# Kernel tuning notes

Measured on AMD Instinct MI355X. Metric: run time of the kernel, lower is better.

The kernel has to match this reference:

```python
import jax, jax.numpy as jnp
import numpy as np

N_NODES = 100000


def _mean_agg(x, src, dst, n_nodes):
    # gather neighbor (src) features, segment-sum into destination nodes, divide by in-degree
    summed = jax.ops.segment_sum(x[src], dst, num_segments=n_nodes)  # [N, d]
    deg = jax.ops.segment_sum(jnp.ones_like(dst, dtype=x.dtype), dst, num_segments=n_nodes)
    return summed / jnp.clip(deg, 1.0)[:, None]  # DGL clamps zero in-degree to 1


def _sage_conv(x, src, dst, W_self, W_neigh, b, n_nodes):
    h_neigh = _mean_agg(x, src, dst, n_nodes)
    # DGL SAGEConv(mean): fc_self(h_self) + fc_neigh(h_neigh); single bias
    return x @ W_self + h_neigh @ W_neigh + b


def setup_inputs() -> dict:
    key = jax.random.key(0)
    ks = jax.random.split(key, 8)
    in_f, hid_f, out_f = 64, 64, 16
    n_edges = 1200000
    return {
        "x": jax.random.normal(ks[0], (N_NODES, in_f), dtype=jnp.float32),
        "src": jax.random.randint(ks[1], (n_edges,), 0, N_NODES),
        "dst": jax.random.randint(ks[2], (n_edges,), 0, N_NODES),
        "W1_self": jax.random.normal(ks[3], (in_f, hid_f), dtype=jnp.float32) / np.sqrt(in_f),
        "W1_neigh": jax.random.normal(ks[4], (in_f, hid_f), dtype=jnp.float32) / np.sqrt(in_f),
        "b1": jnp.zeros((hid_f,), dtype=jnp.float32),
        "W2_self": jax.random.normal(ks[5], (hid_f, out_f), dtype=jnp.float32) / np.sqrt(hid_f),
        "W2_neigh": jax.random.normal(ks[6], (hid_f, out_f), dtype=jnp.float32) / np.sqrt(hid_f),
        "b2": jnp.zeros((out_f,), dtype=jnp.float32),
    }


def reference(x, src, dst, W1_self, W1_neigh, b1, W2_self, W2_neigh, b2):
    h = _sage_conv(x, src, dst, W1_self, W1_neigh, b1, N_NODES)
    h = jax.nn.relu(h)
    h = _sage_conv(h, src, dst, W2_self, W2_neigh, b2, N_NODES)
    return h
```

## Files before the change

### kernel.cpp

```cpp
#include <hip/hip_runtime.h>

#define N_NODES 100000
#define N_EDGES 1200000
#define BK 64
#define NB 1563
#define CHUNK_E 4096
#define NBLK_E 293
#define TOT_H (NB * NBLK_E)
#define NSB2 ((TOT_H + 1023) / 1024)
#define CAP 1536
#define ND1 3125

#define OFF_ROWPTR 0
#define OFF_HISTG  401408
#define OFF_BLK2   2234368
#define OFF_PAIRS  2236416
#define OFF_SORTED 7036928
#define OFF_Y1     11837440
#define OFF_H1     24637440

typedef __attribute__((ext_vector_type(8))) short short8;
typedef __attribute__((ext_vector_type(4))) float f32x4;

__device__ __forceinline__ unsigned short f2bf(float f) {
    unsigned u = __float_as_uint(f);
    unsigned r = (u + 0x7fffu + ((u >> 16) & 1u)) >> 16;
    return (unsigned short)r;
}

__global__ __launch_bounds__(256) void wtrans_kernel(
    const float* __restrict__ Wn, unsigned short* __restrict__ wt)
{
    const int t = threadIdx.x;
#pragma unroll
    for (int i = 0; i < 16; ++i) {
        const int e = t + i * 256;
        wt[(e & 63) * 64 + (e >> 6)] = f2bf(Wn[e]);
    }
}

__global__ __launch_bounds__(256) void hist_dense1_kernel(
    const int* __restrict__ dst, int* __restrict__ hist_g,
    const float* __restrict__ x,
    const unsigned short* __restrict__ wt,
    const float* __restrict__ Ws, const float* __restrict__ b,
    unsigned short* __restrict__ y1, float* __restrict__ z1)
{
    __shared__ float sx[32 * 64];
    __shared__ unsigned short sxbf[32 * 64];
    const int t = threadIdx.x;

    if (blockIdx.x < NBLK_E) {
        int* h = (int*)sx;
        const int e0 = blockIdx.x * CHUNK_E;
        const int e1 = min(e0 + CHUNK_E, N_EDGES);
        for (int i = t; i < NB; i += 256) h[i] = 0;
        __syncthreads();
        for (int e = e0 + t; e < e1; e += 256)
            atomicAdd(&h[dst[e] >> 6], 1);
        __syncthreads();
        for (int i = t; i < NB; i += 256)
            hist_g[i * NBLK_E + blockIdx.x] = h[i];
        return;
    }

    const int bid = blockIdx.x - NBLK_E;
    const int w = t >> 6;
    const int lane = t & 63;
    const int chunk = bid * 32;

    {
        const float4* gx = (const float4*)(x + (size_t)chunk * 64);
        float4* sx4 = (float4*)sx;
#pragma unroll
        for (int i = 0; i < 2; ++i) {
            const int fidx = t + i * 256;
            const float4 v = gx[fidx];
            sx4[fidx] = v;
            const int r = fidx >> 4;
            const int f = fidx & 15;
            const int cs = (f >> 1) ^ (r & 7);
            uint2 p;
            p.x = (unsigned)f2bf(v.x) | ((unsigned)f2bf(v.y) << 16);
            p.y = (unsigned)f2bf(v.z) | ((unsigned)f2bf(v.w) << 16);
            *(uint2*)((char*)sxbf + r * 128 + cs * 16 + (f & 1) * 8) = p;
        }
    }
    __syncthreads();

    if (w >= 2) {
        const int nsub = (w & 1) * 16;
        float wr[64];
#pragma unroll
        for (int k = 0; k < 64; ++k) wr[k] = Ws[k * 64 + lane];
        const float bj = b[lane];
#pragma unroll 1
        for (int m = 0; m < 16; ++m) {
            const int node = nsub + m;
            const float4* xr = (const float4*)(sx + node * 64);
            float a0 = 0.f, a1 = 0.f, a2 = 0.f, a3 = 0.f;
#pragma unroll
            for (int k4 = 0; k4 < 16; ++k4) {
                float4 v = xr[k4];
                a0 += v.x * wr[4 * k4 + 0];
                a1 += v.y * wr[4 * k4 + 1];
                a2 += v.z * wr[4 * k4 + 2];
                a3 += v.w * wr[4 * k4 + 3];
            }
            z1[(size_t)(chunk + node) * 64 + lane] = (a0 + a1) + (a2 + a3) + bj;
        }
    } else {
        const int n0 = (w & 1) * 16;
        const int row = lane & 15;
        const int kg = lane >> 4;
        short8 af[2];
#pragma unroll
        for (int kt = 0; kt < 2; ++kt) {
            const int cs = (kt * 4 + kg) ^ (row & 7);
            af[kt] = *(const short8*)((const char*)sxbf + (n0 + row) * 128 + cs * 16);
        }
        f32x4 acc[4];
#pragma unroll
        for (int nt = 0; nt < 4; ++nt) acc[nt] = (f32x4){0.f, 0.f, 0.f, 0.f};
#pragma unroll
        for (int nt = 0; nt < 4; ++nt) {
            const short8* wrow = (const short8*)(wt + (nt * 16 + row) * 64);
#pragma unroll
            for (int kt = 0; kt < 2; ++kt) {
                const short8 bf = wrow[kt * 4 + kg];
                acc[nt] = __builtin_amdgcn_mfma_f32_16x16x32_bf16(
                    af[kt], bf, acc[nt], 0, 0, 0);
            }
        }
#pragma unroll
        for (int nt = 0; nt < 4; ++nt)
#pragma unroll
            for (int r = 0; r < 4; ++r) {
                const int node = n0 + 4 * kg + r;
                y1[(size_t)(chunk + node) * 64 + nt * 16 + row] = f2bf(acc[nt][r]);
            }
    }
}

__global__ __launch_bounds__(1024) void scan2_blocks_kernel(
    int* __restrict__ hist_g, int* __restrict__ blk2)
{
    __shared__ int s[1024];
    int i = blockIdx.x * 1024 + threadIdx.x;
    int v = (i < TOT_H) ? hist_g[i] : 0;
    s[threadIdx.x] = v;
    __syncthreads();
    for (int off = 1; off < 1024; off <<= 1) {
        int tv = (threadIdx.x >= off) ? s[threadIdx.x - off] : 0;
        __syncthreads();
        s[threadIdx.x] += tv;
        __syncthreads();
    }
    if (i < TOT_H) hist_g[i] = s[threadIdx.x] - v;
    if (threadIdx.x == 1023) blk2[blockIdx.x] = s[1023];
}

__device__ __forceinline__ void local_tops_scan(const int* blk2, int* tops, int t)
{
    int v = (t < NSB2) ? blk2[t] : 0;
    tops[t] = v;
    __syncthreads();
    for (int off = 1; off < 512; off <<= 1) {
        int tv = (t >= off) ? tops[t - off] : 0;
        __syncthreads();
        tops[t] += tv;
        __syncthreads();
    }
    int ex = tops[t] - v;
    __syncthreads();
    tops[t] = ex;
    __syncthreads();
}

__global__ __launch_bounds__(512) void pair_scatter_kernel(
    const int* __restrict__ src, const int* __restrict__ dst,
    const int* __restrict__ hs_scan, const int* __restrict__ blk2,
    unsigned* __restrict__ pairs)
{
    __shared__ int base_s[NB];
    __shared__ int cur_s[NB];
    __shared__ int tops[512];
    const int b = blockIdx.x;
    const int t = threadIdx.x;
    const int e0 = b * CHUNK_E;
    const int e1 = min(e0 + CHUNK_E, N_EDGES);

    local_tops_scan(blk2, tops, t);

    for (int i = t; i < NB; i += 512) {
        int idx = i * NBLK_E + b;
        base_s[i] = hs_scan[idx] + tops[idx >> 10];
        cur_s[i] = 0;
    }
    __syncthreads();
    for (int e = e0 + t; e < e1; e += 512) {
        int d = dst[e];
        int bk = d >> 6;
        int pos = base_s[bk] + atomicAdd(&cur_s[bk], 1);
        pairs[pos] = ((unsigned)src[e] << 6) | (unsigned)(d & 63);
    }
}

__global__ __launch_bounds__(512) void fused_gather1_kernel(
    const unsigned short* __restrict__ y1,
    const unsigned* __restrict__ pairs,
    const int* __restrict__ hs_scan, const int* __restrict__ blk2,
    int* __restrict__ row_ptr, int* __restrict__ sorted_src,
    float* __restrict__ h1)
{
    __shared__ int slist[CAP];
    __shared__ int hist[BK];
    __shared__ int sc[BK];
    __shared__ int cur[BK];
    __shared__ int tops[512];
    const int b = blockIdx.x;
    const int t = threadIdx.x;

    local_tops_scan(blk2, tops, t);

    const int i0 = b * NBLK_E;
    const int start = hs_scan[i0] + tops[i0 >> 10];
    const int end = (b == NB - 1) ? N_EDGES
                    : hs_scan[i0 + NBLK_E] + tops[(i0 + NBLK_E) >> 10];
    const int cnt = end - start;
    const int node0 = b * BK;

    if (t < BK) hist[t] = 0;
    __syncthreads();
    for (int e = start + t; e < end; e += 512)
        atomicAdd(&hist[pairs[e] & 63u], 1);
    __syncthreads();

    int v = (t < BK) ? hist[t] : 0;
    if (t < BK) sc[t] = v;
    __syncthreads();
    for (int off = 1; off < BK; off <<= 1) {
        int tv = (t >= off && t < BK) ? sc[t - off] : 0;
        __syncthreads();
        if (t < BK) sc[t] += tv;
        __syncthreads();
    }
    const int excl = (t < BK) ? sc[t] - v : 0;
    if (t < BK && node0 + t < N_NODES) row_ptr[node0 + t] = start + excl;
    if (b == NB - 1 && t == 0) row_ptr[N_NODES] = N_EDGES;
    if (t < BK) cur[t] = excl;
    __syncthreads();

    const int wv = t >> 6;
    const int lane = t & 63;
    const int sub = lane >> 5;
    const int sl = lane & 31;
    const int eg = sl >> 3;
    const int fl = sl & 7;

    if (cnt <= CAP) {
        for (int e = start + t; e < end; e += 512) {
            unsigned u = pairs[e];
            int p = atomicAdd(&cur[u & 63u], 1);
            slist[p] = (int)(u >> 6);
        }
        __syncthreads();
        for (int i = t; i < cnt; i += 512)
            sorted_src[start + i] = slist[i];
        for (int q = 0; q < 4; ++q) {
            const int node = wv * 8 + q * 2 + sub;
            const int gn = node0 + node;
            if (gn >= N_NODES) break;
            const int o = sc[node] - hist[node];
            const int dg = hist[node];
            float4* hp = (float4*)(h1 + (size_t)gn * 64);
            float4 z;
            if (eg < 2) z = hp[fl * 2 + eg];
            float a0 = 0.f, a1 = 0.f, a2 = 0.f, a3 = 0.f;
            float a4 = 0.f, a5 = 0.f, a6 = 0.f, a7 = 0.f;
            for (int base = 0; base < dg; base += 8) {
                const int i0e = base + eg;
                const int i1e = base + 4 + eg;
                const bool v0 = i0e < dg, v1 = i1e < dg;
                uint4 r0, r1;
                if (v0) {
                    const int s = slist[o + i0e];
                    r0 = ((const uint4*)(y1 + (size_t)s * 64))[fl];
                }
                if (v1) {
                    const int s = slist[o + i1e];
                    r1 = ((const uint4*)(y1 + (size_t)s * 64))[fl];
                }
                if (v0) {
                    a0 += __uint_as_float(r0.x << 16);
                    a1 += __uint_as_float(r0.x & 0xffff0000u);
                    a2 += __uint_as_float(r0.y << 16);
                    a3 += __uint_as_float(r0.y & 0xffff0000u);
                    a4 += __uint_as_float(r0.z << 16);
                    a5 += __uint_as_float(r0.z & 0xffff0000u);
                    a6 += __uint_as_float(r0.w << 16);
                    a7 += __uint_as_float(r0.w & 0xffff0000u);
                }
                if (v1) {
                    a0 += __uint_as_float(r1.x << 16);
                    a1 += __uint_as_float(r1.x & 0xffff0000u);
                    a2 += __uint_as_float(r1.y << 16);
                    a3 += __uint_as_float(r1.y & 0xffff0000u);
                    a4 += __uint_as_float(r1.z << 16);
                    a5 += __uint_as_float(r1.z & 0xffff0000u);
                    a6 += __uint_as_float(r1.w << 16);
                    a7 += __uint_as_float(r1.w & 0xffff0000u);
                }
            }
#pragma unroll
            for (int d = 8; d <= 16; d <<= 1) {
                a0 += __shfl_xor(a0, d); a1 += __shfl_xor(a1, d);
                a2 += __shfl_xor(a2, d); a3 += __shfl_xor(a3, d);
                a4 += __shfl_xor(a4, d); a5 += __shfl_xor(a5, d);
                a6 += __shfl_xor(a6, d); a7 += __shfl_xor(a7, d);
            }
            const float invd = 1.0f / (float)max(dg, 1);
            if (eg == 0) {
                hp[fl * 2] = make_float4(fmaxf(z.x + a0 * invd, 0.f),
                                         fmaxf(z.y + a1 * invd, 0.f),
                                         fmaxf(z.z + a2 * invd, 0.f),
                                         fmaxf(z.w + a3 * invd, 0.f));
            } else if (eg == 1) {
                hp[fl * 2 + 1] = make_float4(fmaxf(z.x + a4 * invd, 0.f),
                                             fmaxf(z.y + a5 * invd, 0.f),
                                             fmaxf(z.z + a6 * invd, 0.f),
                                             fmaxf(z.w + a7 * invd, 0.f));
            }
        }
    } else {
        if (t < BK) cur[t] = start + excl;
        __syncthreads();
        for (int e = start + t; e < end; e += 512) {
            unsigned u = pairs[e];
            int p = atomicAdd(&cur[u & 63u], 1);
            sorted_src[p] = (int)(u >> 6);
        }
        __syncthreads();
        for (int q = 0; q < 4; ++q) {
            const int node = wv * 8 + q * 2 + sub;
            const int gn = node0 + node;
            if (gn >= N_NODES) break;
            const int o = start + sc[node] - hist[node];
            const int dg = hist[node];
            float4* hp = (float4*)(h1 + (size_t)gn * 64);
            float4 z;
            if (eg < 2) z = hp[fl * 2 + eg];
            float a0 = 0.f, a1 = 0.f, a2 = 0.f, a3 = 0.f;
            float a4 = 0.f, a5 = 0.f, a6 = 0.f, a7 = 0.f;
            for (int base = 0; base < dg; base += 4) {
                const int idx = base + eg;
                if (idx < dg) {
                    const int s = sorted_src[o + idx];
                    uint4 raw = ((const uint4*)(y1 + (size_t)s * 64))[fl];
                    a0 += __uint_as_float(raw.x << 16);
                    a1 += __uint_as_float(raw.x & 0xffff0000u);
                    a2 += __uint_as_float(raw.y << 16);
                    a3 += __uint_as_float(raw.y & 0xffff0000u);
                    a4 += __uint_as_float(raw.z << 16);
                    a5 += __uint_as_float(raw.z & 0xffff0000u);
                    a6 += __uint_as_float(raw.w << 16);
                    a7 += __uint_as_float(raw.w & 0xffff0000u);
                }
            }
#pragma unroll
            for (int d = 8; d <= 16; d <<= 1) {
                a0 += __shfl_xor(a0, d); a1 += __shfl_xor(a1, d);
                a2 += __shfl_xor(a2, d); a3 += __shfl_xor(a3, d);
                a4 += __shfl_xor(a4, d); a5 += __shfl_xor(a5, d);
                a6 += __shfl_xor(a6, d); a7 += __shfl_xor(a7, d);
            }
            const float invd = 1.0f / (float)max(dg, 1);
            if (eg == 0) {
                hp[fl * 2] = make_float4(fmaxf(z.x + a0 * invd, 0.f),
                                         fmaxf(z.y + a1 * invd, 0.f),
                                         fmaxf(z.z + a2 * invd, 0.f),
                                         fmaxf(z.w + a3 * invd, 0.f));
            } else if (eg == 1) {
                hp[fl * 2 + 1] = make_float4(fmaxf(z.x + a4 * invd, 0.f),
                                             fmaxf(z.y + a5 * invd, 0.f),
                                             fmaxf(z.z + a6 * invd, 0.f),
                                             fmaxf(z.w + a7 * invd, 0.f));
            }
        }
    }
}

__global__ __launch_bounds__(256) void dense2_kernel(
    const float* __restrict__ h1,
    const float* __restrict__ Wn, const float* __restrict__ Ws,
    const float* __restrict__ b,
    float* __restrict__ y2, float* __restrict__ out)
{
    __shared__ float sx[32 * 68];
    const int t = threadIdx.x;
    const int w = t >> 6;
    const int lane = t & 63;
    const int half = w >> 1;
    const int nsub = (w & 1) * 16;
    const int j = lane & 15;
    const int g = lane >> 4;
    const int chunk = blockIdx.x * 32;

    {
        const float4* gx = (const float4*)(h1 + (size_t)chunk * 64);
        float4* sx4 = (float4*)sx;
        int r0 = t >> 4, c0 = t & 15;
        sx4[r0 * 17 + c0] = gx[t];
        sx4[(r0 + 16) * 17 + c0] = gx[t + 256];
    }

    const float* W = half ? Ws : Wn;
    float wr[64];
#pragma unroll
    for (int k = 0; k < 64; ++k) wr[k] = W[k * 16 + j];
    const float bj = half ? b[j] : 0.f;

    __syncthreads();

#pragma unroll 1
    for (int q = 0; q < 4; ++q) {
        const int node = nsub + q * 4 + g;
        const float4* xr = (const float4*)(sx + node * 68);
        float a0 = 0.f, a1 = 0.f, a2 = 0.f, a3 = 0.f;
#pragma unroll
        for (int k4 = 0; k4 < 16; ++k4) {
            float4 v = xr[k4];
            a0 += v.x * wr[4 * k4 + 0];
            a1 += v.y * wr[4 * k4 + 1];
            a2 += v.z * wr[4 * k4 + 2];
            a3 += v.w * wr[4 * k4 + 3];
        }
        const float o = (a0 + a1) + (a2 + a3) + bj;
        const size_t gn = (size_t)(chunk + node);
        if (half) out[gn * 16 + j] = o;
        else      y2[gn * 16 + j] = o;
    }
}

__global__ __launch_bounds__(256) void gather2_kernel(
    const float* __restrict__ y2,
    const int* __restrict__ row_ptr,
    const int* __restrict__ sorted_src,
    float* __restrict__ out)
{
    const int wv = threadIdx.x >> 6;
    const int lane = threadIdx.x & 63;
    const int sub = lane >> 4;
    const int sl = lane & 15;
    const int eg = sl >> 2;
    const int fl = sl & 3;

    const int n = blockIdx.x * 16 + wv * 4 + sub;
    const int start = row_ptr[n];
    const int deg = row_ptr[n + 1] - start;

    float4* op = (float4*)(out + (size_t)n * 16);
    float4 z;
    if (eg == 0) z = op[fl];

    float4 acc = make_float4(0.f, 0.f, 0.f, 0.f);
    for (int base = 0; base < deg; base += 16) {
        int eid = 0;
        if (base + sl < deg) eid = sorted_src[start + base + sl];
#pragma unroll
        for (int jj = 0; jj < 16; jj += 4) {
            const int idx = jj + eg;
            const int s = __shfl(eid, sub * 16 + idx);
            if (base + idx < deg) {
                float4 v = ((const float4*)(y2 + (size_t)s * 16))[fl];
                acc.x += v.x; acc.y += v.y; acc.z += v.z; acc.w += v.w;
            }
        }
    }
#pragma unroll
    for (int d = 4; d <= 8; d <<= 1) {
        acc.x += __shfl_xor(acc.x, d); acc.y += __shfl_xor(acc.y, d);
        acc.z += __shfl_xor(acc.z, d); acc.w += __shfl_xor(acc.w, d);
    }
    const float invd = 1.0f / (float)max(deg, 1);
    if (eg == 0) {
        op[fl] = make_float4(z.x + acc.x * invd, z.y + acc.y * invd,
                             z.z + acc.z * invd, z.w + acc.w * invd);
    }
}

extern "C" void kernel_launch(void* const* d_in, const int* in_sizes, int n_in,
                              void* d_out, int out_size, void* d_ws, size_t ws_size,
                              hipStream_t stream) {
    const float* x   = (const float*)d_in[0];
    const int*   src = (const int*)d_in[1];
    const int*   dst = (const int*)d_in[2];
    const float* W1s = (const float*)d_in[3];
    const float* W1n = (const float*)d_in[4];
    const float* b1  = (const float*)d_in[5];
    const float* W2s = (const float*)d_in[6];
    const float* W2n = (const float*)d_in[7];
    const float* b2  = (const float*)d_in[8];
    float* out = (float*)d_out;

    char* ws = (char*)d_ws;
    int* row_ptr    = (int*)(ws + OFF_ROWPTR);
    int* hist_g     = (int*)(ws + OFF_HISTG);
    int* blk2       = (int*)(ws + OFF_BLK2);
    unsigned* pairs = (unsigned*)(ws + OFF_PAIRS);
    unsigned short* wt = (unsigned short*)(ws + OFF_PAIRS);
    int* sorted_src = (int*)(ws + OFF_SORTED);
    unsigned short* y1 = (unsigned short*)(ws + OFF_Y1);
    float* y2       = (float*)(ws + OFF_Y1);
    float* h1       = (float*)(ws + OFF_H1);

    wtrans_kernel<<<1, 256, 0, stream>>>(W1n, wt);
    hist_dense1_kernel<<<NBLK_E + ND1, 256, 0, stream>>>(
        dst, hist_g, x, wt, W1s, b1, y1, h1);
    scan2_blocks_kernel<<<NSB2, 1024, 0, stream>>>(hist_g, blk2);
    pair_scatter_kernel<<<NBLK_E, 512, 0, stream>>>(src, dst, hist_g, blk2, pairs);
    fused_gather1_kernel<<<NB, 512, 0, stream>>>(y1, pairs, hist_g, blk2,
                                                 row_ptr, sorted_src, h1);
    dense2_kernel<<<ND1, 256, 0, stream>>>(h1, W2n, W2s, b2, y2, out);
    gather2_kernel<<<N_NODES / 16, 256, 0, stream>>>(y2, row_ptr, sorted_src, out);
}
```

Before: 237.1 us.

## Split dense1 into separate self and MFMA blocks, hoist tops scan to kernel

The dense1 work is split into two block types: FP32 self-projection blocks that use all four waves on 32 nodes, and separate MFMA neighbor-projection blocks that handle 64 nodes each with bounds checks. The shared-memory footprint shrinks and launch bounds request higher occupancy. The block-level tops scan, previously recomputed by every block of pair_scatter and fused_gather1, becomes a single small kernel that writes exclusive offsets into blk2. Some loops get unroll-2 hints, and early breaks become guarded bodies. These changes trade an extra launch and more blocks for less redundant per-block work and better balance.

```diff
diff --git a/kernel.cpp b/kernel.cpp
--- a/kernel.cpp
+++ b/kernel.cpp
@@ -10,6 +10,7 @@
 #define NSB2 ((TOT_H + 1023) / 1024)
 #define CAP 1536
 #define ND1 3125
+#define NDM 1563
 
 #define OFF_ROWPTR 0
 #define OFF_HISTG  401408
@@ -39,15 +40,14 @@
     }
 }
 
-__global__ __launch_bounds__(256) void hist_dense1_kernel(
+__global__ __launch_bounds__(256, 6) void hist_dense1_kernel(
     const int* __restrict__ dst, int* __restrict__ hist_g,
     const float* __restrict__ x,
     const unsigned short* __restrict__ wt,
     const float* __restrict__ Ws, const float* __restrict__ b,
     unsigned short* __restrict__ y1, float* __restrict__ z1)
 {
-    __shared__ float sx[32 * 64];
-    __shared__ unsigned short sxbf[32 * 64];
+    __shared__ float sx[2048];
     const int t = threadIdx.x;
 
     if (blockIdx.x < NBLK_E) {
@@ -64,38 +64,26 @@
         return;
     }
 
-    const int bid = blockIdx.x - NBLK_E;
-    const int w = t >> 6;
-    const int lane = t & 63;
-    const int chunk = bid * 32;
-
-    {
-        const float4* gx = (const float4*)(x + (size_t)chunk * 64);
-        float4* sx4 = (float4*)sx;
-#pragma unroll
-        for (int i = 0; i < 2; ++i) {
-            const int fidx = t + i * 256;
-            const float4 v = gx[fidx];
-            sx4[fidx] = v;
-            const int r = fidx >> 4;
-            const int f = fidx & 15;
-            const int cs = (f >> 1) ^ (r & 7);
-            uint2 p;
-            p.x = (unsigned)f2bf(v.x) | ((unsigned)f2bf(v.y) << 16);
-            p.y = (unsigned)f2bf(v.z) | ((unsigned)f2bf(v.w) << 16);
-            *(uint2*)((char*)sxbf + r * 128 + cs * 16 + (f & 1) * 8) = p;
-        }
-    }
-    __syncthreads();
-
-    if (w >= 2) {
-        const int nsub = (w & 1) * 16;
+    if (blockIdx.x < NBLK_E + ND1) {
+        const int bid = blockIdx.x - NBLK_E;
+        const int w = t >> 6;
+        const int lane = t & 63;
+        const int chunk = bid * 32;
+        {
+            const float4* gx = (const float4*)(x + (size_t)chunk * 64);
+            float4* sx4 = (float4*)sx;
+            sx4[t] = gx[t];
+            sx4[t + 256] = gx[t + 256];
+        }
         float wr[64];
 #pragma unroll
         for (int k = 0; k < 64; ++k) wr[k] = Ws[k * 64 + lane];
         const float bj = b[lane];
-#pragma unroll 1
-        for (int m = 0; m < 16; ++m) {
+        __syncthreads();
+
+        const int nsub = w * 8;
+#pragma unroll 2
+        for (int m = 0; m < 8; ++m) {
             const int node = nsub + m;
             const float4* xr = (const float4*)(sx + node * 64);
             float a0 = 0.f, a1 = 0.f, a2 = 0.f, a3 = 0.f;
@@ -109,37 +97,62 @@
             }
             z1[(size_t)(chunk + node) * 64 + lane] = (a0 + a1) + (a2 + a3) + bj;
         }
-    } else {
-        const int n0 = (w & 1) * 16;
-        const int row = lane & 15;
-        const int kg = lane >> 4;
-        short8 af[2];
+        return;
+    }
+
+    const int bid = blockIdx.x - NBLK_E - ND1;
+    const int chunk = bid * 64;
+    unsigned short* sxbf = (unsigned short*)sx;
+    {
+        const float4* gx = (const float4*)(x + (size_t)chunk * 64);
+#pragma unroll
+        for (int i = 0; i < 4; ++i) {
+            const int fidx = t + i * 256;
+            const int r = fidx >> 4;
+            const int f = fidx & 15;
+            float4 v = make_float4(0.f, 0.f, 0.f, 0.f);
+            if (chunk + r < N_NODES) v = gx[fidx];
+            const int cs = (f >> 1) ^ (r & 7);
+            uint2 p;
+            p.x = (unsigned)f2bf(v.x) | ((unsigned)f2bf(v.y) << 16);
+            p.y = (unsigned)f2bf(v.z) | ((unsigned)f2bf(v.w) << 16);
+            *(uint2*)((char*)sxbf + r * 128 + cs * 16 + (f & 1) * 8) = p;
+        }
+    }
+    __syncthreads();
+
+    const int w = t >> 6;
+    const int lane = t & 63;
+    const int n0 = w * 16;
+    const int row = lane & 15;
+    const int kg = lane >> 4;
+    short8 af[2];
+#pragma unroll
+    for (int kt = 0; kt < 2; ++kt) {
+        const int cs = (kt * 4 + kg) ^ (row & 7);
+        af[kt] = *(const short8*)((const char*)sxbf + (n0 + row) * 128 + cs * 16);
+    }
+    f32x4 acc[4];
+#pragma unroll
+    for (int nt = 0; nt < 4; ++nt) acc[nt] = (f32x4){0.f, 0.f, 0.f, 0.f};
+#pragma unroll
+    for (int nt = 0; nt < 4; ++nt) {
+        const short8* wrow = (const short8*)(wt + (nt * 16 + row) * 64);
 #pragma unroll
         for (int kt = 0; kt < 2; ++kt) {
-            const int cs = (kt * 4 + kg) ^ (row & 7);
-            af[kt] = *(const short8*)((const char*)sxbf + (n0 + row) * 128 + cs * 16);
-        }
-        f32x4 acc[4];
-#pragma unroll
-        for (int nt = 0; nt < 4; ++nt) acc[nt] = (f32x4){0.f, 0.f, 0.f, 0.f};
-#pragma unroll
-        for (int nt = 0; nt < 4; ++nt) {
-            const short8* wrow = (const short8*)(wt + (nt * 16 + row) * 64);
-#pragma unroll
-            for (int kt = 0; kt < 2; ++kt) {
-                const short8 bf = wrow[kt * 4 + kg];
-                acc[nt] = __builtin_amdgcn_mfma_f32_16x16x32_bf16(
-                    af[kt], bf, acc[nt], 0, 0, 0);
-            }
-        }
-#pragma unroll
-        for (int nt = 0; nt < 4; ++nt)
-#pragma unroll
-            for (int r = 0; r < 4; ++r) {
-                const int node = n0 + 4 * kg + r;
-                y1[(size_t)(chunk + node) * 64 + nt * 16 + row] = f2bf(acc[nt][r]);
-            }
-    }
+            acc[nt] = __builtin_amdgcn_mfma_f32_16x16x32_bf16(
+                af[kt], wrow[kt * 4 + kg], acc[nt], 0, 0, 0);
+        }
+    }
+#pragma unroll
+    for (int nt = 0; nt < 4; ++nt)
+#pragma unroll
+        for (int r = 0; r < 4; ++r) {
+            const int node = n0 + 4 * kg + r;
+            const int gn = chunk + node;
+            if (gn < N_NODES)
+                y1[(size_t)gn * 64 + nt * 16 + row] = f2bf(acc[nt][r]);
+        }
 }
 
 __global__ __launch_bounds__(1024) void scan2_blocks_kernel(
@@ -160,21 +173,20 @@
     if (threadIdx.x == 1023) blk2[blockIdx.x] = s[1023];
 }
 
-__device__ __forceinline__ void local_tops_scan(const int* blk2, int* tops, int t)
-{
+__global__ __launch_bounds__(512) void tops_scan_kernel(int* __restrict__ blk2)
+{
+    __shared__ int s[512];
+    const int t = threadIdx.x;
     int v = (t < NSB2) ? blk2[t] : 0;
-    tops[t] = v;
+    s[t] = v;
     __syncthreads();
     for (int off = 1; off < 512; off <<= 1) {
-        int tv = (t >= off) ? tops[t - off] : 0;
-        __syncthreads();
-        tops[t] += tv;
-        __syncthreads();
-    }
-    int ex = tops[t] - v;
-    __syncthreads();
-    tops[t] = ex;
-    __syncthreads();
+        int tv = (t >= off) ? s[t - off] : 0;
+        __syncthreads();
+        s[t] += tv;
+        __syncthreads();
+    }
+    if (t < NSB2) blk2[t] = s[t] - v;
 }
 
 __global__ __launch_bounds__(512) void pair_scatter_kernel(
@@ -184,17 +196,14 @@
 {
     __shared__ int base_s[NB];
     __shared__ int cur_s[NB];
-    __shared__ int tops[512];
     const int b = blockIdx.x;
     const int t = threadIdx.x;
     const int e0 = b * CHUNK_E;
     const int e1 = min(e0 + CHUNK_E, N_EDGES);
 
-    local_tops_scan(blk2, tops, t);
-
     for (int i = t; i < NB; i += 512) {
         int idx = i * NBLK_E + b;
-        base_s[i] = hs_scan[idx] + tops[idx >> 10];
+        base_s[i] = hs_scan[idx] + blk2[idx >> 10];
         cur_s[i] = 0;
     }
     __syncthreads();
@@ -217,16 +226,13 @@
     __shared__ int hist[BK];
     __shared__ int sc[BK];
     __shared__ int cur[BK];
-    __shared__ int tops[512];
     const int b = blockIdx.x;
     const int t = threadIdx.x;
 
-    local_tops_scan(blk2, tops, t);
-
     const int i0 = b * NBLK_E;
-    const int start = hs_scan[i0] + tops[i0 >> 10];
+    const int start = hs_scan[i0] + blk2[i0 >> 10];
     const int end = (b == NB - 1) ? N_EDGES
-                    : hs_scan[i0 + NBLK_E] + tops[(i0 + NBLK_E) >> 10];
+                    : hs_scan[i0 + NBLK_E] + blk2[(i0 + NBLK_E) >> 10];
     const int cnt = end - start;
     const int node0 = b * BK;
 
@@ -267,10 +273,11 @@
         __syncthreads();
         for (int i = t; i < cnt; i += 512)
             sorted_src[start + i] = slist[i];
+#pragma unroll 2
         for (int q = 0; q < 4; ++q) {
             const int node = wv * 8 + q * 2 + sub;
             const int gn = node0 + node;
-            if (gn >= N_NODES) break;
+            if (gn < N_NODES) {
             const int o = sc[node] - hist[node];
             const int dg = hist[node];
             float4* hp = (float4*)(h1 + (size_t)gn * 64);
@@ -331,6 +338,7 @@
                                              fmaxf(z.z + a6 * invd, 0.f),
                                              fmaxf(z.w + a7 * invd, 0.f));
             }
+            }
         }
     } else {
         if (t < BK) cur[t] = start + excl;
@@ -344,7 +352,7 @@
         for (int q = 0; q < 4; ++q) {
             const int node = wv * 8 + q * 2 + sub;
             const int gn = node0 + node;
-            if (gn >= N_NODES) break;
+            if (gn < N_NODES) {
             const int o = start + sc[node] - hist[node];
             const int dg = hist[node];
             float4* hp = (float4*)(h1 + (size_t)gn * 64);
@@ -386,6 +394,7 @@
                                              fmaxf(z.z + a6 * invd, 0.f),
                                              fmaxf(z.w + a7 * invd, 0.f));
             }
+            }
         }
     }
 }
@@ -422,7 +431,7 @@
 
     __syncthreads();
 
-#pragma unroll 1
+#pragma unroll 2
     for (int q = 0; q < 4; ++q) {
         const int node = nsub + q * 4 + g;
         const float4* xr = (const float4*)(sx + node * 68);
@@ -515,9 +524,10 @@
     float* h1       = (float*)(ws + OFF_H1);
 
     wtrans_kernel<<<1, 256, 0, stream>>>(W1n, wt);
-    hist_dense1_kernel<<<NBLK_E + ND1, 256, 0, stream>>>(
+    hist_dense1_kernel<<<NBLK_E + ND1 + NDM, 256, 0, stream>>>(
         dst, hist_g, x, wt, W1s, b1, y1, h1);
     scan2_blocks_kernel<<<NSB2, 1024, 0, stream>>>(hist_g, blk2);
+    tops_scan_kernel<<<1, 512, 0, stream>>>(blk2);
     pair_scatter_kernel<<<NBLK_E, 512, 0, stream>>>(src, dst, hist_g, blk2, pairs);
     fused_gather1_kernel<<<NB, 512, 0, stream>>>(y1, pairs, hist_g, blk2,
                                                  row_ptr, sorted_src, h1);
```

After: 546.3 us. 130% more time.
